# Optimization experiments

Measured on AMD Instinct MI355X. Metric: run time of the kernel, lower is better.

## Reference

```python
import jax, jax.numpy as jnp
import numpy as np
from jax import lax

SPAN = 11
K = 2 * SPAN + 1          # 23 -> 529 offsets
SIG_RGB = 0.1
SIG_XY = 6.0
LAM = 0.15
B, C, H, W = 2, 3, 160, 160


def _patches(x):
    """x: (N, C, H, W) -> (N, C, K, K, H, W), zero-padded.
    patch[di, dj] at pixel (i, j) equals x[i + di - SPAN, j + dj - SPAN],
    matching the torch module's shifted-slice double loop (dx = di - SPAN)."""
    n, c, h, w = x.shape
    xp = jnp.pad(x, ((0, 0), (0, 0), (SPAN, SPAN), (SPAN, SPAN)))

    def get(off):
        di = off // K
        dj = off % K
        return lax.dynamic_slice(xp, (0, 0, di, dj), (n, c, h, w))

    p = jax.vmap(get)(jnp.arange(K * K))              # (K*K, N, C, H, W)
    return p.reshape(K, K, n, c, h, w).transpose(2, 3, 0, 1, 4, 5)


def setup_inputs() -> dict:
    key = jax.random.key(0)
    k1, k2, k3, k4, k5 = jax.random.split(key, 5)
    logit = jax.random.normal(k1, (B, C, H, W), jnp.float32)
    target = jax.random.randint(k2, (B, H, W), 0, C)
    # small-magnitude image so exp(-0.5*(x - patch/0.1)^2) does not fully underflow
    image = jax.random.uniform(k3, (B, 3, H, W), jnp.float32) * 0.1
    source_map = (jax.random.uniform(k4, (B, 1, H, W)) > 0.5).astype(jnp.float32)
    destination_map = (jax.random.uniform(k5, (B, H, W)) > 0.5).astype(jnp.float32)
    return dict(logit=logit, target=target, image=image,
                source_map=source_map, destination_map=destination_map)


def _gcrf(image, y_hat, source_map, m_dst):
    b, c, h, w = y_hat.shape
    img_p = _patches(image)                                  # (B,3,K,K,H,W)
    valid = _patches(jnp.ones((1, 1, h, w), image.dtype))[0, 0]  # (K,K,H,W) in-bounds mask
    # NOTE: faithful to source bug: only the shifted feature is divided by sigma
    drgb = image[:, :, None, None] - img_p / SIG_RGB
    k_rgb = jnp.exp(-0.5 * jnp.sum(drgb * drgb, axis=1))     # (B,K,K,H,W)
    ii, jj = jnp.meshgrid(jnp.arange(h, dtype=image.dtype),
                          jnp.arange(w, dtype=image.dtype), indexing='ij')
    idx = jnp.stack([ii, jj])[None]                          # (1,2,H,W)
    idx_p = _patches(idx)[0]                                 # (2,K,K,H,W)
    dxy = idx[0][:, None, None] - idx_p / SIG_XY
    k_xy = jnp.exp(-0.5 * jnp.sum(dxy * dxy, axis=0))        # (K,K,H,W)
    kmat = (k_rgb + k_xy[None]) * valid[None]                # out-of-bounds offsets stay 0
    m_src = _patches(source_map)[:, 0]                       # (B,K,K,H,W)
    Kg = kmat * m_src * m_dst[:, None, None]                 # gated kernel
    U = _patches(y_hat)                                      # (B,C,K,K,H,W)
    Egy = jnp.einsum('bcijhw,bijhw->bchw', U, Kg)            # sum over window
    temp = jnp.einsum('bchw,bdhw->bcd', Egy, y_hat)          # (B,C,C)
    Moff = 1.0 - jnp.eye(c, dtype=y_hat.dtype)               # off-diagonal compatibility
    return jnp.sum(Moff * temp) / (b * h * w)


def reference(logit, target, image, source_map, destination_map):
    y_hat = jax.nn.softmax(logit, axis=1)
    m_dst = 1.0 - destination_map
    L_gcrf = _gcrf(image, y_hat, source_map, m_dst)
    logp = jax.nn.log_softmax(logit, axis=1)
    L_ce = -jnp.take_along_axis(logp, target[:, None], axis=1)[:, 0]  # (B,H,W)
    L_ce = jnp.mean(L_ce * destination_map)
    return L_ce + LAM * L_gcrf
```

## Files before the change

kernel.cpp:

```cpp
#include <hip/hip_runtime.h>

#define Bn 2
#define Cn 3
#define Hn 160
#define Wn 160
#define SPANc 11
#define Kc 23
#define HWn (Hn * Wn)
#define PW 182
#define PP (PW * PW)
#define LAMc 0.15f
#define TJ 32
#define Gc 4
#define TI 32
#define NROW (TI + Kc - 1)
#define NREC (NROW * TJ)
#define CEXP (-0.72134752f)
#define NPREP ((Bn * PP + 255) / 256)

__device__ __forceinline__ float wave_reduce64(float v) {
#pragma unroll
    for (int off = 32; off > 0; off >>= 1) v += __shfl_down(v, off, 64);
    return v;
}

__global__ __launch_bounds__(256) void prep_kernel(
    const float* __restrict__ logit, const int* __restrict__ target,
    const float* __restrict__ image, const float* __restrict__ srcmap,
    const float* __restrict__ dstmap, float4* __restrict__ gA,
    float2* __restrict__ gB, float4* __restrict__ cvec,
    float* __restrict__ pc, double* __restrict__ acc)
{
    int idx = blockIdx.x * 256 + threadIdx.x;
    float ce = 0.0f;
    if (idx < Bn * PP) {
        int b   = idx / PP;
        int rem = idx - b * PP;
        int ip  = rem / PW;
        int jp  = rem - ip * PW;
        int i = ip - SPANc, j = jp - SPANc;
        if ((unsigned)i < (unsigned)Hn && (unsigned)j < (unsigned)Wn) {
            int r = i * Wn + j;
            int p = b * HWn + r;
            const float* lg = logit + (size_t)b * Cn * HWn + r;
            float l0 = lg[0], l1 = lg[HWn], l2 = lg[2 * HWn];
            float m = fmaxf(l0, fmaxf(l1, l2));
            float e0 = __expf(l0 - m), e1 = __expf(l1 - m), e2 = __expf(l2 - m);
            float s = e0 + e1 + e2;
            float inv = 1.0f / s;
            float y0 = e0 * inv, y1 = e1 * inv, y2 = e2 * inv;
            float lse = m + __logf(s);

            const float* im = image + (size_t)b * 3 * HWn + r;
            float i0v = im[0], i1v = im[HWn], i2v = im[2 * HWn];
            float sv = srcmap[p];
            float dv = dstmap[p];

            gA[idx] = make_float4(i0v, i1v, i2v, sv * y0);
            gB[idx] = make_float2(sv * y1, sv * y2);

            float md = LAMc * (1.0f - dv);
            cvec[p] = make_float4(md * (1.0f - y0), md * (1.0f - y1),
                                  md * (1.0f - y2), 0.0f);

            int t = target[p];
            float lt = (t == 0) ? l0 : ((t == 1) ? l1 : l2);
            ce = (lse - lt) * dv;
        } else {
            gA[idx] = make_float4(0.f, 0.f, 0.f, 0.f);
            gB[idx] = make_float2(0.f, 0.f);
        }
    }
    if (idx == 0) *acc = 0.0;

    float v = wave_reduce64(ce);
    __shared__ float wsum[4];
    int tid = threadIdx.x;
    if ((tid & 63) == 0) wsum[tid >> 6] = v;
    __syncthreads();
    if (tid == 0) pc[blockIdx.x] = wsum[0] + wsum[1] + wsum[2] + wsum[3];
}

__device__ __forceinline__ void tap(const float4 pa, const float2 pb,
                                    float cA0, float cA1, float cA2,
                                    bool xy_on, float dy2, float dxv,
                                    float& e0, float& e1, float& e2)
{
    float d0 = fmaf(pa.x, -10.0f, cA0);
    float d1 = fmaf(pa.y, -10.0f, cA1);
    float d2 = fmaf(pa.z, -10.0f, cA2);
    float ss = fmaf(d0, d0, fmaf(d1, d1, d2 * d2));
    float k = exp2f(ss * CEXP);
    if (xy_on) k += exp2f(fmaf(dxv, dxv, dy2) * CEXP);
    e0 = fmaf(k, pa.w, e0);
    e1 = fmaf(k, pb.x, e1);
    e2 = fmaf(k, pb.y, e2);
}

__global__ __launch_bounds__(256) void gcrf_kernel(
    const float4* __restrict__ gA, const float2* __restrict__ gB,
    const float4* __restrict__ cvec, double* __restrict__ acc)
{
    __shared__ float4 sA[NREC];
    __shared__ float2 sB[NREC];

    int tx = threadIdx.x;
    int ty = threadIdx.y;
    int tid = ty * TJ + tx;
    int jx = blockIdx.x;
    int j  = jx * TJ + tx;
    int by = blockIdx.y;
    int b  = by / 5;
    int it = by - b * 5;
    int i0g = it * TI + ty * Gc;
    int dj = blockIdx.z;

    size_t g0 = (size_t)b * PP + (size_t)(it * TI) * PW + (jx * TJ + dj);
    for (int n = tid; n < NREC; n += 256) {
        int rr = n >> 5, cc = n & 31;
        size_t gi = g0 + (size_t)rr * PW + cc;
        sA[n] = gA[gi];
        sB[n] = gB[gi];
    }
    __syncthreads();

    int lbase = ty * Gc * TJ + tx;
    float cA0[Gc], cA1[Gc], cA2[Gc];
#pragma unroll
    for (int c = 0; c < Gc; ++c) {
        float4 cr = sA[lbase + (c + SPANc) * TJ];
        cA0[c] = cr.x; cA1[c] = cr.y; cA2[c] = cr.z;
    }

    bool xy_on = (j < 16) && (i0g < 16);
    float dy = (float)j - (float)(j + dj - SPANc) * (1.0f / 6.0f);
    float dy2 = dy * dy;
    float fi0 = (float)i0g;

    float eg[Gc][3];
#pragma unroll
    for (int c = 0; c < Gc; ++c) { eg[c][0] = 0.f; eg[c][1] = 0.f; eg[c][2] = 0.f; }

#pragma unroll
    for (int r = 0; r < 3; ++r) {
        float4 pa = sA[lbase + r * TJ];
        float2 pb = sB[lbase + r * TJ];
        float fpi = fi0 + (float)(r - SPANc);
#pragma unroll
        for (int c = 0; c < 3; ++c) {
            if (c > r) continue;
            tap(pa, pb, cA0[c], cA1[c], cA2[c], xy_on, dy2,
                fi0 + (float)c - fpi * (1.0f / 6.0f), eg[c][0], eg[c][1], eg[c][2]);
        }
    }
#pragma unroll 2
    for (int r = 3; r <= 22; ++r) {
        float4 pa = sA[lbase + r * TJ];
        float2 pb = sB[lbase + r * TJ];
        float fpi = fi0 + (float)(r - SPANc);
#pragma unroll
        for (int c = 0; c < Gc; ++c) {
            tap(pa, pb, cA0[c], cA1[c], cA2[c], xy_on, dy2,
                fi0 + (float)c - fpi * (1.0f / 6.0f), eg[c][0], eg[c][1], eg[c][2]);
        }
    }
#pragma unroll
    for (int r = 23; r <= 25; ++r) {
        float4 pa = sA[lbase + r * TJ];
        float2 pb = sB[lbase + r * TJ];
        float fpi = fi0 + (float)(r - SPANc);
#pragma unroll
        for (int c = 1; c < Gc; ++c) {
            if (c < r - 22) continue;
            tap(pa, pb, cA0[c], cA1[c], cA2[c], xy_on, dy2,
                fi0 + (float)c - fpi * (1.0f / 6.0f), eg[c][0], eg[c][1], eg[c][2]);
        }
    }

    const float4* cv = cvec + ((size_t)b * HWn + (size_t)i0g * Wn + j);
    float contrib = 0.0f;
#pragma unroll
    for (int c = 0; c < Gc; ++c) {
        float4 t = cv[(size_t)c * Wn];
        contrib += eg[c][0] * t.x + eg[c][1] * t.y + eg[c][2] * t.z;
    }

    float v = wave_reduce64(contrib);
    __shared__ float wsum[4];
    if ((tid & 63) == 0) wsum[tid >> 6] = v;
    __syncthreads();
    if (tid == 0) atomicAdd(acc, (double)(wsum[0] + wsum[1] + wsum[2] + wsum[3]));
}

__global__ __launch_bounds__(256) void finalize_kernel(
    const float* __restrict__ pc, const double* __restrict__ acc,
    float* __restrict__ out)
{
    int t = threadIdx.x;
    float s = 0.0f;
    if (t < NPREP) s += pc[t];
    if (t + 256 < NPREP) s += pc[t + 256];
    float v = wave_reduce64(s);
    __shared__ float wsum[4];
    if ((t & 63) == 0) wsum[t >> 6] = v;
    __syncthreads();
    if (t == 0) {
        double tot = acc[0] + (double)(wsum[0] + wsum[1] + wsum[2] + wsum[3]);
        out[0] = (float)(tot * (1.0 / (double)(Bn * HWn)));
    }
}

extern "C" void kernel_launch(void* const* d_in, const int* in_sizes, int n_in,
                              void* d_out, int out_size, void* d_ws, size_t ws_size,
                              hipStream_t stream)
{
    const float* logit  = (const float*)d_in[0];
    const int*   target = (const int*)d_in[1];
    const float* image  = (const float*)d_in[2];
    const float* srcmap = (const float*)d_in[3];
    const float* dstmap = (const float*)d_in[4];
    float* out = (float*)d_out;

    const size_t NRECG = (size_t)Bn * PP;
    double* acc  = (double*)d_ws;
    float*  pc   = (float*)((char*)d_ws + 256);
    float4* gA   = (float4*)((char*)d_ws + 4096);
    float2* gB   = (float2*)((char*)d_ws + 4096 + NRECG * 16);
    float4* cvec = (float4*)((char*)d_ws + 4096 + NRECG * 24);

    prep_kernel<<<NPREP, 256, 0, stream>>>(logit, target, image, srcmap, dstmap,
                                           gA, gB, cvec, pc, acc);
    dim3 grid(Wn / TJ, (Hn / TI) * Bn, Kc);
    dim3 blk(TJ, 8);
    gcrf_kernel<<<grid, blk, 0, stream>>>(gA, gB, cvec, acc);
    finalize_kernel<<<1, 256, 0, stream>>>(pc, acc, out);
}
```

Measured before the change: 92.15 us.

## Split vertical window across two blocks and fold finalize into gcrf last block

Each gcrf block now handles half of the 23 vertical offsets (12 or 11 rows), doubling the grid to 46 z-slices and halving the shared-memory staging per block. This raises occupancy and the number of blocks in flight. The finalize kernel is removed: the last block to finish, found through an atomic counter, sums the prep partials and writes the output, saving one launch. In exchange the inner row loop now has a runtime trip count with a per-tap bounds check instead of fully specialised edge loops, and the centre pixels are read from global memory.

Measured after the change: 124.8 us. 35.5% more time.

```diff
diff --git a/kernel.cpp b/kernel.cpp
--- a/kernel.cpp
+++ b/kernel.cpp
@@ -13,10 +13,11 @@
 #define TJ 32
 #define Gc 4
 #define TI 32
-#define NROW (TI + Kc - 1)
-#define NREC (NROW * TJ)
+#define NROWMAX (TI + 12 - 1)
+#define NRECMAX (NROWMAX * TJ)
 #define CEXP (-0.72134752f)
 #define NPREP ((Bn * PP + 255) / 256)
+#define NBLK (5 * 10 * 46)
 
 __device__ __forceinline__ float wave_reduce64(float v) {
 #pragma unroll
@@ -29,7 +30,8 @@
     const float* __restrict__ image, const float* __restrict__ srcmap,
     const float* __restrict__ dstmap, float4* __restrict__ gA,
     float2* __restrict__ gB, float4* __restrict__ cvec,
-    float* __restrict__ pc, double* __restrict__ acc)
+    float* __restrict__ pc, double* __restrict__ acc,
+    unsigned int* __restrict__ counter)
 {
     int idx = blockIdx.x * 256 + threadIdx.x;
     float ce = 0.0f;
@@ -71,7 +73,7 @@
             gB[idx] = make_float2(0.f, 0.f);
         }
     }
-    if (idx == 0) *acc = 0.0;
+    if (idx == 0) { *acc = 0.0; *counter = 0u; }
 
     float v = wave_reduce64(ce);
     __shared__ float wsum[4];
@@ -99,10 +101,12 @@
 
 __global__ __launch_bounds__(256) void gcrf_kernel(
     const float4* __restrict__ gA, const float2* __restrict__ gB,
-    const float4* __restrict__ cvec, double* __restrict__ acc)
-{
-    __shared__ float4 sA[NREC];
-    __shared__ float2 sB[NREC];
+    const float4* __restrict__ cvec, const float* __restrict__ pc,
+    double* __restrict__ acc, unsigned int* __restrict__ counter,
+    float* __restrict__ out)
+{
+    __shared__ float4 sA[NRECMAX];
+    __shared__ float2 sB[NRECMAX];
 
     int tx = threadIdx.x;
     int ty = threadIdx.y;
@@ -113,10 +117,15 @@
     int b  = by / 5;
     int it = by - b * 5;
     int i0g = it * TI + ty * Gc;
-    int dj = blockIdx.z;
-
-    size_t g0 = (size_t)b * PP + (size_t)(it * TI) * PW + (jx * TJ + dj);
-    for (int n = tid; n < NREC; n += 256) {
+    int bz = blockIdx.z;
+    int dj   = bz >> 1;
+    int half = bz & 1;
+    int d0 = half * 12;
+    int nd = 12 - half;
+
+    int nrec = (TI + nd - 1) * TJ;
+    size_t g0 = (size_t)b * PP + (size_t)(it * TI + d0) * PW + (jx * TJ + dj);
+    for (int n = tid; n < nrec; n += 256) {
         int rr = n >> 5, cc = n & 31;
         size_t gi = g0 + (size_t)rr * PW + cc;
         sA[n] = gA[gi];
@@ -124,12 +133,15 @@
     }
     __syncthreads();
 
-    int lbase = ty * Gc * TJ + tx;
+    int lty = ty * Gc;
     float cA0[Gc], cA1[Gc], cA2[Gc];
-#pragma unroll
-    for (int c = 0; c < Gc; ++c) {
-        float4 cr = sA[lbase + (c + SPANc) * TJ];
-        cA0[c] = cr.x; cA1[c] = cr.y; cA2[c] = cr.z;
+    {
+        size_t crow = (size_t)b * PP + (size_t)(i0g + SPANc) * PW + (j + SPANc);
+#pragma unroll
+        for (int c = 0; c < Gc; ++c) {
+            float4 cr = gA[crow + (size_t)c * PW];
+            cA0[c] = cr.x; cA1[c] = cr.y; cA2[c] = cr.z;
+        }
     }
 
     bool xy_on = (j < 16) && (i0g < 16);
@@ -141,39 +153,18 @@
 #pragma unroll
     for (int c = 0; c < Gc; ++c) { eg[c][0] = 0.f; eg[c][1] = 0.f; eg[c][2] = 0.f; }
 
-#pragma unroll
-    for (int r = 0; r < 3; ++r) {
+    int lbase = lty * TJ + tx;
+    for (int r = 0; r < nd + Gc - 1; ++r) {
         float4 pa = sA[lbase + r * TJ];
         float2 pb = sB[lbase + r * TJ];
-        float fpi = fi0 + (float)(r - SPANc);
-#pragma unroll
-        for (int c = 0; c < 3; ++c) {
-            if (c > r) continue;
-            tap(pa, pb, cA0[c], cA1[c], cA2[c], xy_on, dy2,
-                fi0 + (float)c - fpi * (1.0f / 6.0f), eg[c][0], eg[c][1], eg[c][2]);
-        }
-    }
-#pragma unroll 2
-    for (int r = 3; r <= 22; ++r) {
-        float4 pa = sA[lbase + r * TJ];
-        float2 pb = sB[lbase + r * TJ];
-        float fpi = fi0 + (float)(r - SPANc);
+        float fpi = fi0 + (float)(r + d0 - SPANc);
 #pragma unroll
         for (int c = 0; c < Gc; ++c) {
-            tap(pa, pb, cA0[c], cA1[c], cA2[c], xy_on, dy2,
-                fi0 + (float)c - fpi * (1.0f / 6.0f), eg[c][0], eg[c][1], eg[c][2]);
-        }
-    }
-#pragma unroll
-    for (int r = 23; r <= 25; ++r) {
-        float4 pa = sA[lbase + r * TJ];
-        float2 pb = sB[lbase + r * TJ];
-        float fpi = fi0 + (float)(r - SPANc);
-#pragma unroll
-        for (int c = 1; c < Gc; ++c) {
-            if (c < r - 22) continue;
-            tap(pa, pb, cA0[c], cA1[c], cA2[c], xy_on, dy2,
-                fi0 + (float)c - fpi * (1.0f / 6.0f), eg[c][0], eg[c][1], eg[c][2]);
+            if ((unsigned)(r - c) < (unsigned)nd) {
+                tap(pa, pb, cA0[c], cA1[c], cA2[c], xy_on, dy2,
+                    fi0 + (float)c - fpi * (1.0f / 6.0f),
+                    eg[c][0], eg[c][1], eg[c][2]);
+            }
         }
     }
 
@@ -187,26 +178,28 @@
 
     float v = wave_reduce64(contrib);
     __shared__ float wsum[4];
+    __shared__ int lastflag;
     if ((tid & 63) == 0) wsum[tid >> 6] = v;
     __syncthreads();
-    if (tid == 0) atomicAdd(acc, (double)(wsum[0] + wsum[1] + wsum[2] + wsum[3]));
-}
-
-__global__ __launch_bounds__(256) void finalize_kernel(
-    const float* __restrict__ pc, const double* __restrict__ acc,
-    float* __restrict__ out)
-{
-    int t = threadIdx.x;
-    float s = 0.0f;
-    if (t < NPREP) s += pc[t];
-    if (t + 256 < NPREP) s += pc[t + 256];
-    float v = wave_reduce64(s);
-    __shared__ float wsum[4];
-    if ((t & 63) == 0) wsum[t >> 6] = v;
-    __syncthreads();
-    if (t == 0) {
-        double tot = acc[0] + (double)(wsum[0] + wsum[1] + wsum[2] + wsum[3]);
-        out[0] = (float)(tot * (1.0 / (double)(Bn * HWn)));
+    if (tid == 0) {
+        atomicAdd(acc, (double)(wsum[0] + wsum[1] + wsum[2] + wsum[3]));
+        __threadfence();
+        unsigned int old = atomicAdd(counter, 1u);
+        lastflag = (old == NBLK - 1) ? 1 : 0;
+    }
+    __syncthreads();
+    if (lastflag) {
+        float s = 0.0f;
+        if (tid < NPREP) s += pc[tid];
+        if (tid + 256 < NPREP) s += pc[tid + 256];
+        float v2 = wave_reduce64(s);
+        if ((tid & 63) == 0) wsum[tid >> 6] = v2;
+        __syncthreads();
+        if (tid == 0) {
+            double tot = atomicAdd(acc, 0.0);
+            tot += (double)(wsum[0] + wsum[1] + wsum[2] + wsum[3]);
+            out[0] = (float)(tot * (1.0 / (double)(Bn * HWn)));
+        }
     }
 }
 
@@ -222,16 +215,16 @@
     float* out = (float*)d_out;
 
     const size_t NRECG = (size_t)Bn * PP;
-    double* acc  = (double*)d_ws;
-    float*  pc   = (float*)((char*)d_ws + 256);
-    float4* gA   = (float4*)((char*)d_ws + 4096);
-    float2* gB   = (float2*)((char*)d_ws + 4096 + NRECG * 16);
-    float4* cvec = (float4*)((char*)d_ws + 4096 + NRECG * 24);
+    double*       acc     = (double*)d_ws;
+    unsigned int* counter = (unsigned int*)((char*)d_ws + 128);
+    float*        pc      = (float*)((char*)d_ws + 256);
+    float4*       gA      = (float4*)((char*)d_ws + 4096);
+    float2*       gB      = (float2*)((char*)d_ws + 4096 + NRECG * 16);
+    float4*       cvec    = (float4*)((char*)d_ws + 4096 + NRECG * 24);
 
     prep_kernel<<<NPREP, 256, 0, stream>>>(logit, target, image, srcmap, dstmap,
-                                           gA, gB, cvec, pc, acc);
-    dim3 grid(Wn / TJ, (Hn / TI) * Bn, Kc);
+                                           gA, gB, cvec, pc, acc, counter);
+    dim3 grid(Wn / TJ, (Hn / TI) * Bn, 46);
     dim3 blk(TJ, 8);
-    gcrf_kernel<<<grid, blk, 0, stream>>>(gA, gB, cvec, acc);
-    finalize_kernel<<<1, 256, 0, stream>>>(pc, acc, out);
-}
+    gcrf_kernel<<<grid, blk, 0, stream>>>(gA, gB, cvec, pc, acc, counter, out);
+}
```

## Pack gCRF patch features as bf16 and fold the RGB scale into the exponent

Applied to the files above, without the earlier changes.

The prep kernel now stores the image channels and source-gated softmax probabilities as packed bf16 (12 bytes per record instead of 24), halving global and LDS traffic for the patch tiles. The image values are prescaled by sqrt(0.5*log2 e) so the RGB exponent becomes exp2(-ss), which drops one multiply per tap. The gcrf kernel also gets a launch_bounds occupancy hint of 4 blocks. In exchange every tap does bit unpacking of the bf16 values, and bf16 rounding lowers the accuracy of both the squared-difference exponent and the weights.

After: 91.43 us. About the same (-0.8%).

```diff
diff --git a/kernel.cpp b/kernel.cpp
--- a/kernel.cpp
+++ b/kernel.cpp
@@ -16,19 +16,27 @@
 #define NROW (TI + Kc - 1)
 #define NREC (NROW * TJ)
 #define CEXP (-0.72134752f)
+#define SRGB_S (0.84932190f)
 #define NPREP ((Bn * PP + 255) / 256)
 
 __device__ __forceinline__ float wave_reduce64(float v) {
 #pragma unroll
     for (int off = 32; off > 0; off >>= 1) v += __shfl_down(v, off, 64);
     return v;
+}
+
+__device__ __forceinline__ unsigned int bf16pk(float a, float b) {
+    unsigned int ua = __float_as_uint(a), ub = __float_as_uint(b);
+    ua += 0x7fffu + ((ua >> 16) & 1u);
+    ub += 0x7fffu + ((ub >> 16) & 1u);
+    return (ua & 0xffff0000u) | (ub >> 16);
 }
 
 __global__ __launch_bounds__(256) void prep_kernel(
     const float* __restrict__ logit, const int* __restrict__ target,
     const float* __restrict__ image, const float* __restrict__ srcmap,
-    const float* __restrict__ dstmap, float4* __restrict__ gA,
-    float2* __restrict__ gB, float4* __restrict__ cvec,
+    const float* __restrict__ dstmap, uint2* __restrict__ gU2,
+    unsigned int* __restrict__ gU1, float4* __restrict__ cvec,
     float* __restrict__ pc, double* __restrict__ acc)
 {
     int idx = blockIdx.x * 256 + threadIdx.x;
@@ -52,12 +60,12 @@
             float lse = m + __logf(s);
 
             const float* im = image + (size_t)b * 3 * HWn + r;
-            float i0v = im[0], i1v = im[HWn], i2v = im[2 * HWn];
+            float i0v = im[0] * SRGB_S, i1v = im[HWn] * SRGB_S, i2v = im[2 * HWn] * SRGB_S;
             float sv = srcmap[p];
             float dv = dstmap[p];
 
-            gA[idx] = make_float4(i0v, i1v, i2v, sv * y0);
-            gB[idx] = make_float2(sv * y1, sv * y2);
+            gU2[idx] = make_uint2(bf16pk(i0v, i1v), bf16pk(i2v, sv * y0));
+            gU1[idx] = bf16pk(sv * y1, sv * y2);
 
             float md = LAMc * (1.0f - dv);
             cvec[p] = make_float4(md * (1.0f - y0), md * (1.0f - y1),
@@ -67,8 +75,8 @@
             float lt = (t == 0) ? l0 : ((t == 1) ? l1 : l2);
             ce = (lse - lt) * dv;
         } else {
-            gA[idx] = make_float4(0.f, 0.f, 0.f, 0.f);
-            gB[idx] = make_float2(0.f, 0.f);
+            gU2[idx] = make_uint2(0u, 0u);
+            gU1[idx] = 0u;
         }
     }
     if (idx == 0) *acc = 0.0;
@@ -81,28 +89,29 @@
     if (tid == 0) pc[blockIdx.x] = wsum[0] + wsum[1] + wsum[2] + wsum[3];
 }
 
-__device__ __forceinline__ void tap(const float4 pa, const float2 pb,
+__device__ __forceinline__ void tap(float p0, float p1, float p2,
+                                    float q0, float q1, float q2,
                                     float cA0, float cA1, float cA2,
                                     bool xy_on, float dy2, float dxv,
                                     float& e0, float& e1, float& e2)
 {
-    float d0 = fmaf(pa.x, -10.0f, cA0);
-    float d1 = fmaf(pa.y, -10.0f, cA1);
-    float d2 = fmaf(pa.z, -10.0f, cA2);
+    float d0 = fmaf(p0, -10.0f, cA0);
+    float d1 = fmaf(p1, -10.0f, cA1);
+    float d2 = fmaf(p2, -10.0f, cA2);
     float ss = fmaf(d0, d0, fmaf(d1, d1, d2 * d2));
-    float k = exp2f(ss * CEXP);
+    float k = exp2f(-ss);
     if (xy_on) k += exp2f(fmaf(dxv, dxv, dy2) * CEXP);
-    e0 = fmaf(k, pa.w, e0);
-    e1 = fmaf(k, pb.x, e1);
-    e2 = fmaf(k, pb.y, e2);
-}
-
-__global__ __launch_bounds__(256) void gcrf_kernel(
-    const float4* __restrict__ gA, const float2* __restrict__ gB,
+    e0 = fmaf(k, q0, e0);
+    e1 = fmaf(k, q1, e1);
+    e2 = fmaf(k, q2, e2);
+}
+
+__global__ __launch_bounds__(256, 4) void gcrf_kernel(
+    const uint2* __restrict__ gU2, const unsigned int* __restrict__ gU1,
     const float4* __restrict__ cvec, double* __restrict__ acc)
 {
-    __shared__ float4 sA[NREC];
-    __shared__ float2 sB[NREC];
+    __shared__ uint2 sU2[NREC];
+    __shared__ unsigned int sU1[NREC];
 
     int tx = threadIdx.x;
     int ty = threadIdx.y;
@@ -119,8 +128,8 @@
     for (int n = tid; n < NREC; n += 256) {
         int rr = n >> 5, cc = n & 31;
         size_t gi = g0 + (size_t)rr * PW + cc;
-        sA[n] = gA[gi];
-        sB[n] = gB[gi];
+        sU2[n] = gU2[gi];
+        sU1[n] = gU1[gi];
     }
     __syncthreads();
 
@@ -128,8 +137,10 @@
     float cA0[Gc], cA1[Gc], cA2[Gc];
 #pragma unroll
     for (int c = 0; c < Gc; ++c) {
-        float4 cr = sA[lbase + (c + SPANc) * TJ];
-        cA0[c] = cr.x; cA1[c] = cr.y; cA2[c] = cr.z;
+        uint2 cu = sU2[lbase + (c + SPANc) * TJ];
+        cA0[c] = __uint_as_float(cu.x & 0xffff0000u);
+        cA1[c] = __uint_as_float(cu.x << 16);
+        cA2[c] = __uint_as_float(cu.y & 0xffff0000u);
     }
 
     bool xy_on = (j < 16) && (i0g < 16);
@@ -143,36 +154,54 @@
 
 #pragma unroll
     for (int r = 0; r < 3; ++r) {
-        float4 pa = sA[lbase + r * TJ];
-        float2 pb = sB[lbase + r * TJ];
+        uint2 ru = sU2[lbase + r * TJ];
+        unsigned int rv = sU1[lbase + r * TJ];
+        float p0 = __uint_as_float(ru.x & 0xffff0000u);
+        float p1 = __uint_as_float(ru.x << 16);
+        float p2 = __uint_as_float(ru.y & 0xffff0000u);
+        float q0 = __uint_as_float(ru.y << 16);
+        float q1 = __uint_as_float(rv & 0xffff0000u);
+        float q2 = __uint_as_float(rv << 16);
         float fpi = fi0 + (float)(r - SPANc);
 #pragma unroll
         for (int c = 0; c < 3; ++c) {
             if (c > r) continue;
-            tap(pa, pb, cA0[c], cA1[c], cA2[c], xy_on, dy2,
+            tap(p0, p1, p2, q0, q1, q2, cA0[c], cA1[c], cA2[c], xy_on, dy2,
                 fi0 + (float)c - fpi * (1.0f / 6.0f), eg[c][0], eg[c][1], eg[c][2]);
         }
     }
 #pragma unroll 2
     for (int r = 3; r <= 22; ++r) {
-        float4 pa = sA[lbase + r * TJ];
-        float2 pb = sB[lbase + r * TJ];
+        uint2 ru = sU2[lbase + r * TJ];
+        unsigned int rv = sU1[lbase + r * TJ];
+        float p0 = __uint_as_float(ru.x & 0xffff0000u);
+        float p1 = __uint_as_float(ru.x << 16);
+        float p2 = __uint_as_float(ru.y & 0xffff0000u);
+        float q0 = __uint_as_float(ru.y << 16);
+        float q1 = __uint_as_float(rv & 0xffff0000u);
+        float q2 = __uint_as_float(rv << 16);
         float fpi = fi0 + (float)(r - SPANc);
 #pragma unroll
         for (int c = 0; c < Gc; ++c) {
-            tap(pa, pb, cA0[c], cA1[c], cA2[c], xy_on, dy2,
+            tap(p0, p1, p2, q0, q1, q2, cA0[c], cA1[c], cA2[c], xy_on, dy2,
                 fi0 + (float)c - fpi * (1.0f / 6.0f), eg[c][0], eg[c][1], eg[c][2]);
         }
     }
 #pragma unroll
     for (int r = 23; r <= 25; ++r) {
-        float4 pa = sA[lbase + r * TJ];
-        float2 pb = sB[lbase + r * TJ];
+        uint2 ru = sU2[lbase + r * TJ];
+        unsigned int rv = sU1[lbase + r * TJ];
+        float p0 = __uint_as_float(ru.x & 0xffff0000u);
+        float p1 = __uint_as_float(ru.x << 16);
+        float p2 = __uint_as_float(ru.y & 0xffff0000u);
+        float q0 = __uint_as_float(ru.y << 16);
+        float q1 = __uint_as_float(rv & 0xffff0000u);
+        float q2 = __uint_as_float(rv << 16);
         float fpi = fi0 + (float)(r - SPANc);
 #pragma unroll
         for (int c = 1; c < Gc; ++c) {
             if (c < r - 22) continue;
-            tap(pa, pb, cA0[c], cA1[c], cA2[c], xy_on, dy2,
+            tap(p0, p1, p2, q0, q1, q2, cA0[c], cA1[c], cA2[c], xy_on, dy2,
                 fi0 + (float)c - fpi * (1.0f / 6.0f), eg[c][0], eg[c][1], eg[c][2]);
         }
     }
@@ -222,16 +251,16 @@
     float* out = (float*)d_out;
 
     const size_t NRECG = (size_t)Bn * PP;
-    double* acc  = (double*)d_ws;
-    float*  pc   = (float*)((char*)d_ws + 256);
-    float4* gA   = (float4*)((char*)d_ws + 4096);
-    float2* gB   = (float2*)((char*)d_ws + 4096 + NRECG * 16);
-    float4* cvec = (float4*)((char*)d_ws + 4096 + NRECG * 24);
+    double*       acc  = (double*)d_ws;
+    float*        pc   = (float*)((char*)d_ws + 256);
+    uint2*        gU2  = (uint2*)((char*)d_ws + 4096);
+    unsigned int* gU1  = (unsigned int*)((char*)d_ws + 4096 + NRECG * 8);
+    float4*       cvec = (float4*)((char*)d_ws + 4096 + NRECG * 12);
 
     prep_kernel<<<NPREP, 256, 0, stream>>>(logit, target, image, srcmap, dstmap,
-                                           gA, gB, cvec, pc, acc);
+                                           gU2, gU1, cvec, pc, acc);
     dim3 grid(Wn / TJ, (Hn / TI) * Bn, Kc);
     dim3 blk(TJ, 8);
-    gcrf_kernel<<<grid, blk, 0, stream>>>(gA, gB, cvec, acc);
+    gcrf_kernel<<<grid, blk, 0, stream>>>(gU2, gU1, cvec, acc);
     finalize_kernel<<<1, 256, 0, stream>>>(pc, acc, out);
 }
```
